# Performance work log

Hardware: AMD Instinct MI355X
Metric: run time of the kernel (lower is better)

## Reference

```python
import jax, jax.numpy as jnp
import numpy as np

IGNORE_LABEL = 255
THRESH = 0.9
MIN_KEPT = 10000


def setup_inputs() -> dict:
    key = jax.random.key(0)
    k1, k2 = jax.random.split(key)
    n, c, d, h, w = 2, 12, 64, 128, 128
    predict = jax.random.normal(k1, (n, c, d, h, w), dtype=jnp.float32)
    target = jax.random.randint(k2, (n, d, h, w), 0, c, dtype=jnp.int64)
    return {"predict": predict, "target": target}


def reference(predict, target):
    n, c, d, h, w = predict.shape
    # rollaxis(predict, 1).reshape(c, -1): class-major flattening, matching target.ravel()
    logits = jnp.moveaxis(predict, 1, 0).reshape(c, -1)          # (c, N)
    labels = target.reshape(-1)                                   # (N,)
    valid = labels != IGNORE_LABEL
    safe_lab = jnp.where(valid, labels, 0)

    logp = jax.nn.log_softmax(logits, axis=0)                     # (c, N), stable softmax
    lp_at_label = jnp.take_along_axis(logp, safe_lab[None, :], axis=0)[0]  # (N,)
    prob_at_label = jnp.exp(lp_at_label)                          # softmax prob of true class

    num_valid = valid.sum()
    # k-th smallest true-class prob among valid pixels (invalid -> +inf pushed to end)
    sorted_prob = jnp.sort(jnp.where(valid, prob_at_label, jnp.inf))
    k_idx = jnp.maximum(jnp.minimum(MIN_KEPT, num_valid) - 1, 0)
    th_val = sorted_prob[k_idx]
    threshold = jnp.maximum(th_val, THRESH)

    # if min_kept >= num_valid: keep all valid; else keep hard examples (prob <= threshold)
    keep_all = MIN_KEPT >= num_valid
    kept = valid & jnp.where(keep_all, True, prob_at_label <= threshold)

    # masked mean cross-entropy (CrossEntropyLoss with ignore_index, mean reduction)
    nll = -lp_at_label
    num = jnp.sum(jnp.where(kept, nll, 0.0))
    cnt = jnp.sum(kept)
    loss = num / jnp.maximum(cnt, 1).astype(nll.dtype)
    return loss
```

## Files before the change

### kernel.cpp

```cpp
#include <hip/hip_runtime.h>
#include <hip/hip_bf16.h>
#include <math.h>


#define IGNORE_LABEL 255
#define MIN_KEPT 10000u

constexpr int   C         = 12;
constexpr int   PIX_SHIFT = 20;
constexpr int   PIX_MASK  = (1 << PIX_SHIFT) - 1;
constexpr int   NBINS     = 2048;
constexpr float BIN_SCALE = (float)NBINS / 0.1f;

struct Ws {
    double       sum_p3;
    unsigned int cnt_p3;
    unsigned int flag;
    float        threshold;
    unsigned int done;
    unsigned int done2;
    unsigned int pad[9];
    unsigned int hist[NBINS];
};

__device__ inline float wave_reduce_f(float v) {
    #pragma unroll
    for (int o = 32; o > 0; o >>= 1) v += __shfl_down(v, o, 64);
    return v;
}
__device__ inline unsigned int wave_reduce_u(unsigned int v) {
    #pragma unroll
    for (int o = 32; o > 0; o >>= 1) v += __shfl_down(v, o, 64);
    return v;
}
__device__ inline double wave_reduce_d(double v) {
    #pragma unroll
    for (int o = 32; o > 0; o >>= 1) v += __shfl_down(v, o, 64);
    return v;
}

__global__ __launch_bounds__(256, 4) void main_pass_kernel(
        const float* __restrict__ pred, const int* __restrict__ tgt,
        Ws* __restrict__ ws, uint4* __restrict__ partials, int npix) {
    const int tid = blockIdx.x * blockDim.x + threadIdx.x;

    float        my_sle = 0.0f, my_sva = 0.0f;
    unsigned int my_cle = 0u,   my_cva = 0u;

    const int p0 = tid << 3;
    if (p0 < npix) {
        const float* base = pred +
            (((size_t)(p0 >> PIX_SHIFT) * C) << PIX_SHIFT) + (p0 & PIX_MASK);
        const int4 la = *(const int4*)(tgt + p0);
        const int4 lb = *(const int4*)(tgt + p0 + 4);
        const int lab[8] = {la.x, la.y, la.z, la.w, lb.x, lb.y, lb.z, lb.w};

        float E[8]  = {0,0,0,0,0,0,0,0};
        float ll[8] = {0,0,0,0,0,0,0,0};
        #pragma unroll
        for (int ci = 0; ci < C; ++ci) {
            const float* csrc = base + ((size_t)ci << PIX_SHIFT);
            const float4 v0 = *(const float4*)(csrc);
            const float4 v1 = *(const float4*)(csrc + 4);
            const float vv[8] = {v0.x, v0.y, v0.z, v0.w, v1.x, v1.y, v1.z, v1.w};
            #pragma unroll
            for (int j = 0; j < 8; ++j) {
                E[j] += __expf(vv[j]);
                if (lab[j] == ci) ll[j] = vv[j];
            }
        }
        #pragma unroll
        for (int j = 0; j < 8; ++j) {
            const float ls   = __logf(E[j]);
            const float nll  = ls - ll[j];
            const float prob = __expf(ll[j] - ls);
            if (lab[j] != IGNORE_LABEL) {
                my_cva += 1u;
                my_sva += nll;
                if (prob <= 0.9f) {
                    my_cle += 1u;
                    my_sle += nll;
                } else {
                    int b = (int)((prob - 0.9f) * BIN_SCALE);
                    b = b < 0 ? 0 : (b >= NBINS - 1 ? NBINS - 1 : b);
                    atomicAdd(&ws->hist[b], 1u);
                }
            }
        }
    }

    __shared__ float        s_le[4], s_va[4];
    __shared__ unsigned int s_cle[4], s_cva[4];
    const int wid = threadIdx.x >> 6, lane = threadIdx.x & 63;
    const float        r_le = wave_reduce_f(my_sle);
    const float        r_va = wave_reduce_f(my_sva);
    const unsigned int r_cl = wave_reduce_u(my_cle);
    const unsigned int r_cv = wave_reduce_u(my_cva);
    if (lane == 0) { s_le[wid] = r_le; s_va[wid] = r_va; s_cle[wid] = r_cl; s_cva[wid] = r_cv; }
    __syncthreads();
    if (threadIdx.x == 0) {
        uint4 p;
        p.x = __float_as_uint(s_le[0] + s_le[1] + s_le[2] + s_le[3]);
        p.y = __float_as_uint(s_va[0] + s_va[1] + s_va[2] + s_va[3]);
        p.z = s_cle[0] + s_cle[1] + s_cle[2] + s_cle[3];
        p.w = s_cva[0] + s_cva[1] + s_cva[2] + s_cva[3];
        partials[blockIdx.x] = p;
    }
}

__global__ __launch_bounds__(1024) void reduce_finalize_kernel(
        Ws* __restrict__ ws, const uint4* __restrict__ partials,
        int nblocks, float* __restrict__ out) {
    double       sle = 0.0, sva = 0.0;
    unsigned int cle = 0u,  cva = 0u;
    for (int i = threadIdx.x; i < nblocks; i += 1024) {
        const uint4 p = partials[i];
        sle += (double)__uint_as_float(p.x);
        sva += (double)__uint_as_float(p.y);
        cle += p.z;
        cva += p.w;
    }
    __shared__ double       d_le[16], d_va[16];
    __shared__ unsigned int u_le[16], u_va[16];
    const int wid = threadIdx.x >> 6, lane = threadIdx.x & 63;
    const double       r_sle = wave_reduce_d(sle);
    const double       r_sva = wave_reduce_d(sva);
    const unsigned int r_cle = wave_reduce_u(cle);
    const unsigned int r_cva = wave_reduce_u(cva);
    if (lane == 0) { d_le[wid] = r_sle; d_va[wid] = r_sva; u_le[wid] = r_cle; u_va[wid] = r_cva; }
    __syncthreads();
    if (threadIdx.x == 0) {
        double       t_sle = 0.0, t_sva = 0.0;
        unsigned int t_cle = 0u,  t_cva = 0u;
        #pragma unroll
        for (int i = 0; i < 16; ++i) {
            t_sle += d_le[i]; t_sva += d_va[i]; t_cle += u_le[i]; t_cva += u_va[i];
        }
        const unsigned int nv = t_cva;
        const unsigned int k  = nv < MIN_KEPT ? nv : MIN_KEPT;
        if (MIN_KEPT >= nv) {
            out[0] = (float)(t_sva / (double)(nv > 0u ? nv : 1u));
            ws->flag = 0u;
        } else if (t_cle >= k) {
            out[0] = (float)(t_sle / (double)(t_cle > 0u ? t_cle : 1u));
            ws->flag = 0u;
        } else {
            unsigned int cum = t_cle;
            int b = NBINS - 1;
            for (int i = 0; i < NBINS; ++i) {
                cum += ws->hist[i];
                if (cum >= k) { b = i; break; }
            }
            ws->threshold = 0.9f + (float)(b + 1) * (0.1f / (float)NBINS);
            ws->flag = 1u;
            out[0] = 0.0f;
        }
    }
}

__global__ __launch_bounds__(256) void fallback_kernel(
        const float* __restrict__ pred, const int* __restrict__ tgt,
        Ws* __restrict__ ws, float* __restrict__ out, int npix_q) {
    if (ws->flag == 0u) return;
    const float th = ws->threshold;
    const int stride = gridDim.x * blockDim.x;

    float        my_s = 0.0f;
    unsigned int my_c = 0u;
    for (int t = blockIdx.x * blockDim.x + threadIdx.x; t < npix_q; t += stride) {
        const int p0 = t << 2;
        const float* base = pred +
            (((size_t)(p0 >> PIX_SHIFT) * C) << PIX_SHIFT) + (p0 & PIX_MASK);
        const int4 li = *(const int4*)(tgt + p0);
        const int lab[4] = {li.x, li.y, li.z, li.w};
        float s[4] = {0,0,0,0}, l_lab[4] = {0,0,0,0};
        #pragma unroll
        for (int ci = 0; ci < C; ++ci) {
            const float4 v = *(const float4*)(base + ((size_t)ci << PIX_SHIFT));
            const float vv[4] = {v.x, v.y, v.z, v.w};
            #pragma unroll
            for (int j = 0; j < 4; ++j) {
                s[j] += __expf(vv[j]);
                if (lab[j] == ci) l_lab[j] = vv[j];
            }
        }
        #pragma unroll
        for (int j = 0; j < 4; ++j) {
            const float ls   = __logf(s[j]);
            const float nll  = ls - l_lab[j];
            const float prob = __expf(l_lab[j] - ls);
            if (lab[j] != IGNORE_LABEL && prob <= th) { my_c += 1u; my_s += nll; }
        }
    }
    __shared__ float        s_s[4];
    __shared__ unsigned int s_c[4];
    const int wid = threadIdx.x >> 6, lane = threadIdx.x & 63;
    const float        r_s = wave_reduce_f(my_s);
    const unsigned int r_c = wave_reduce_u(my_c);
    if (lane == 0) { s_s[wid] = r_s; s_c[wid] = r_c; }
    __syncthreads();
    if (threadIdx.x == 0) {
        const float        t_s = s_s[0] + s_s[1] + s_s[2] + s_s[3];
        const unsigned int t_c = s_c[0] + s_c[1] + s_c[2] + s_c[3];
        if (t_s != 0.0f) atomicAdd(&ws->sum_p3, (double)t_s);
        if (t_c)         atomicAdd(&ws->cnt_p3, t_c);
        __threadfence();
        const unsigned int prev = atomicAdd(&ws->done2, 1u);
        if (prev == gridDim.x - 1u) {
            const unsigned int cnt = ws->cnt_p3;
            out[0] = (float)(ws->sum_p3 / (double)(cnt > 0u ? cnt : 1u));
        }
    }
}

extern "C" void kernel_launch(void* const* d_in, const int* in_sizes, int n_in,
                              void* d_out, int out_size, void* d_ws, size_t ws_size,
                              hipStream_t stream) {
    const float* pred = (const float*)d_in[0];
    const int*   tgt  = (const int*)d_in[1];
    float*       out  = (float*)d_out;
    Ws*          ws   = (Ws*)d_ws;
    uint4*       partials = (uint4*)((char*)d_ws + sizeof(Ws));

    const int npix   = in_sizes[1];
    const int npix_q = npix >> 2;
    const int blocks = (npix / 8 + 255) / 256;

    hipMemsetAsync(d_ws, 0, sizeof(Ws), stream);
    main_pass_kernel<<<blocks, 256, 0, stream>>>(pred, tgt, ws, partials, npix);
    reduce_finalize_kernel<<<1, 1024, 0, stream>>>(ws, partials, blocks, out);
    fallback_kernel<<<128, 256, 0, stream>>>(pred, tgt, ws, out, npix_q);
}
```

Before: 157.9 us.

## Stage logits tile through LDS with direct global-to-LDS async loads

The main pass now has each block load a 1024-pixel by 12-class tile straight into shared memory using global_load_lds, with each wave fetching three class rows, and then computes the softmax statistics from LDS at 4 pixels per thread. The goal is more memory-level parallelism and bulk loads that bypass registers, in place of per-thread float4 global loads of 8 pixels. In exchange it uses 48KB of LDS per block, lowers the occupancy hint to 3, doubles the block count, and assumes npix is a multiple of 1024.

```diff
diff --git a/kernel.cpp b/kernel.cpp
--- a/kernel.cpp
+++ b/kernel.cpp
@@ -9,6 +9,7 @@
 constexpr int   C         = 12;
 constexpr int   PIX_SHIFT = 20;
 constexpr int   PIX_MASK  = (1 << PIX_SHIFT) - 1;
+constexpr int   TILE      = 1024;
 constexpr int   NBINS     = 2048;
 constexpr float BIN_SCALE = (float)NBINS / 0.1f;
 
@@ -39,59 +40,75 @@
     return v;
 }
 
-__global__ __launch_bounds__(256, 4) void main_pass_kernel(
+__device__ inline void gld_lds16(const float* gsrc, float* ldst) {
+    __builtin_amdgcn_global_load_lds(
+        (const __attribute__((address_space(1))) unsigned int*)gsrc,
+        (__attribute__((address_space(3))) unsigned int*)ldst,
+        16, 0, 0);
+}
+
+__global__ __launch_bounds__(256, 3) void main_pass_kernel(
         const float* __restrict__ pred, const int* __restrict__ tgt,
-        Ws* __restrict__ ws, uint4* __restrict__ partials, int npix) {
-    const int tid = blockIdx.x * blockDim.x + threadIdx.x;
+        Ws* __restrict__ ws, uint4* __restrict__ partials) {
+    __shared__ float tileA[C][TILE];
+
+    const int wid  = threadIdx.x >> 6;
+    const int lane = threadIdx.x & 63;
+    const int tile0 = blockIdx.x * TILE;
+    const int ni    = tile0 >> PIX_SHIFT;
+    const int rem   = tile0 & PIX_MASK;
+    const float* nbase = pred + (((size_t)ni * C) << PIX_SHIFT) + rem;
+
+    #pragma unroll
+    for (int cc = 0; cc < 3; ++cc) {
+        const int c = wid * 3 + cc;
+        const float* gsrc = nbase + ((size_t)c << PIX_SHIFT);
+        #pragma unroll
+        for (int k = 0; k < 4; ++k)
+            gld_lds16(gsrc + k * 256 + lane * 4, &tileA[c][k * 256]);
+    }
+
+    const int4 li = *(const int4*)(tgt + tile0 + threadIdx.x * 4);
+    const int lab[4] = {li.x, li.y, li.z, li.w};
+
+    __syncthreads();
+
+    float s[4]     = {0.0f, 0.0f, 0.0f, 0.0f};
+    float l_lab[4] = {0.0f, 0.0f, 0.0f, 0.0f};
+    #pragma unroll
+    for (int c = 0; c < C; ++c) {
+        const float4 v = *(const float4*)&tileA[c][threadIdx.x * 4];
+        const float vv[4] = {v.x, v.y, v.z, v.w};
+        #pragma unroll
+        for (int j = 0; j < 4; ++j) {
+            s[j] += __expf(vv[j]);
+            if (lab[j] == c) l_lab[j] = vv[j];
+        }
+    }
 
     float        my_sle = 0.0f, my_sva = 0.0f;
     unsigned int my_cle = 0u,   my_cva = 0u;
-
-    const int p0 = tid << 3;
-    if (p0 < npix) {
-        const float* base = pred +
-            (((size_t)(p0 >> PIX_SHIFT) * C) << PIX_SHIFT) + (p0 & PIX_MASK);
-        const int4 la = *(const int4*)(tgt + p0);
-        const int4 lb = *(const int4*)(tgt + p0 + 4);
-        const int lab[8] = {la.x, la.y, la.z, la.w, lb.x, lb.y, lb.z, lb.w};
-
-        float E[8]  = {0,0,0,0,0,0,0,0};
-        float ll[8] = {0,0,0,0,0,0,0,0};
-        #pragma unroll
-        for (int ci = 0; ci < C; ++ci) {
-            const float* csrc = base + ((size_t)ci << PIX_SHIFT);
-            const float4 v0 = *(const float4*)(csrc);
-            const float4 v1 = *(const float4*)(csrc + 4);
-            const float vv[8] = {v0.x, v0.y, v0.z, v0.w, v1.x, v1.y, v1.z, v1.w};
-            #pragma unroll
-            for (int j = 0; j < 8; ++j) {
-                E[j] += __expf(vv[j]);
-                if (lab[j] == ci) ll[j] = vv[j];
-            }
-        }
-        #pragma unroll
-        for (int j = 0; j < 8; ++j) {
-            const float ls   = __logf(E[j]);
-            const float nll  = ls - ll[j];
-            const float prob = __expf(ll[j] - ls);
-            if (lab[j] != IGNORE_LABEL) {
-                my_cva += 1u;
-                my_sva += nll;
-                if (prob <= 0.9f) {
-                    my_cle += 1u;
-                    my_sle += nll;
-                } else {
-                    int b = (int)((prob - 0.9f) * BIN_SCALE);
-                    b = b < 0 ? 0 : (b >= NBINS - 1 ? NBINS - 1 : b);
-                    atomicAdd(&ws->hist[b], 1u);
-                }
+    #pragma unroll
+    for (int j = 0; j < 4; ++j) {
+        const float ls   = __logf(s[j]);
+        const float nll  = ls - l_lab[j];
+        const float prob = __expf(l_lab[j] - ls);
+        if (lab[j] != IGNORE_LABEL) {
+            my_cva += 1u;
+            my_sva += nll;
+            if (prob <= 0.9f) {
+                my_cle += 1u;
+                my_sle += nll;
+            } else {
+                int b = (int)((prob - 0.9f) * BIN_SCALE);
+                b = b < 0 ? 0 : (b >= NBINS - 1 ? NBINS - 1 : b);
+                atomicAdd(&ws->hist[b], 1u);
             }
         }
     }
 
     __shared__ float        s_le[4], s_va[4];
     __shared__ unsigned int s_cle[4], s_cva[4];
-    const int wid = threadIdx.x >> 6, lane = threadIdx.x & 63;
     const float        r_le = wave_reduce_f(my_sle);
     const float        r_va = wave_reduce_f(my_sva);
     const unsigned int r_cl = wave_reduce_u(my_cle);
@@ -224,10 +241,10 @@
 
     const int npix   = in_sizes[1];
     const int npix_q = npix >> 2;
-    const int blocks = (npix / 8 + 255) / 256;
+    const int blocks = npix / TILE;
 
     hipMemsetAsync(d_ws, 0, sizeof(Ws), stream);
-    main_pass_kernel<<<blocks, 256, 0, stream>>>(pred, tgt, ws, partials, npix);
+    main_pass_kernel<<<blocks, 256, 0, stream>>>(pred, tgt, ws, partials);
     reduce_finalize_kernel<<<1, 1024, 0, stream>>>(ws, partials, blocks, out);
     fallback_kernel<<<128, 256, 0, stream>>>(pred, tgt, ws, out, npix_q);
 }
```

After: 158.6 us. About the same (+0.4%).
